# Optimization experiments

Measured on AMD Instinct MI355X. Metric: run time of the kernel, lower is better.

Reference implementation:

```python
import jax, jax.numpy as jnp
import numpy as np
import math

B, T, D = 2, 2048, 1024
H = 16
DH = D // H
DFF = 4096
EPS = 1e-5


def setup_inputs() -> dict:
    key = jax.random.key(0)
    ks = jax.random.split(key, 10)
    x = jax.random.normal(ks[0], (B, T, D), dtype=jnp.float32)
    # bool mask, True above diagonal => masked (matches masked_fill semantics)
    causal_mask = jnp.triu(jnp.ones((T, T), dtype=bool), k=1)
    s = 0.02
    return {
        "x": x,
        "causal_mask": causal_mask,
        "gamma1": jnp.ones((D,), jnp.float32),
        "beta1": jnp.zeros((D,), jnp.float32),
        "wq": jax.random.normal(ks[1], (D, D), jnp.float32) * s,
        "wk": jax.random.normal(ks[2], (D, D), jnp.float32) * s,
        "wv": jax.random.normal(ks[3], (D, D), jnp.float32) * s,
        "wo": jax.random.normal(ks[4], (D, D), jnp.float32) * s,
        "gamma2": jnp.ones((D,), jnp.float32),
        "beta2": jnp.zeros((D,), jnp.float32),
        "w1": jax.random.normal(ks[5], (D, DFF), jnp.float32) * s,
        "b1": jnp.zeros((DFF,), jnp.float32),
        "w2": jax.random.normal(ks[6], (DFF, D), jnp.float32) * s,
        "b2": jnp.zeros((D,), jnp.float32),
    }


def _layer_norm(x, gamma, beta):
    mean = jnp.mean(x, axis=-1, keepdims=True)
    var = jnp.mean((x - mean) ** 2, axis=-1, keepdims=True)
    xhat = (x - mean) / jnp.sqrt(var + EPS)
    return gamma * xhat + beta


def _split_heads(x):
    b, t, d = x.shape
    return x.reshape(b, t, H, DH).transpose(0, 2, 1, 3)  # (B,H,T,Dh)


def reference(x, causal_mask, gamma1, beta1, wq, wk, wv, wo,
              gamma2, beta2, w1, b1, w2, b2):
    # --- attention sublayer (pre-LN) ---
    h = _layer_norm(x, gamma1, beta1)
    q = _split_heads(h @ wq)
    k = _split_heads(h @ wk)
    v = _split_heads(h @ wv)
    scores = jnp.einsum('bhqd,bhkd->bhqk', q, k) / math.sqrt(DH)  # (B,H,T,T)
    scores = jnp.where(causal_mask[None, None, :, :], -jnp.inf, scores)
    attn = jax.nn.softmax(scores, axis=-1)
    out = jnp.einsum('bhqk,bhkd->bhqd', attn, v)
    out = out.transpose(0, 2, 1, 3).reshape(x.shape)  # merge heads
    attn_out = out @ wo
    x = x + attn_out
    # --- FFN sublayer (pre-LN) ---
    h = _layer_norm(x, gamma2, beta2)
    ffn = jax.nn.gelu(h @ w1 + b1, approximate=False) @ w2 + b2
    return x + ffn
```

## Files before the change

### kernel.cpp

```cpp
#include <hip/hip_runtime.h>
#include <hip/hip_bf16.h>
#include <math.h>

#define B_   2
#define T_   2048
#define D_   1024
#define H_   16
#define DH_  64
#define DFF_ 4096
#define NTOK (B_*T_)

typedef __attribute__((ext_vector_type(8))) short short8;
typedef __attribute__((ext_vector_type(4))) float f32x4;

static __device__ __forceinline__ short f2bf(float f) {
    union { __hip_bfloat16 h; short s; } u;
    u.h = __float2bfloat16(f);
    return u.s;
}

static __device__ __forceinline__ f32x4 mfma16(short8 a, short8 b, f32x4 c) {
    return __builtin_amdgcn_mfma_f32_16x16x32_bf16(a, b, c, 0, 0, 0);
}

static __device__ __forceinline__ void gload16(const void* g, void* l) {
    __builtin_amdgcn_global_load_lds(
        (__attribute__((address_space(1))) void*)g,
        (__attribute__((address_space(3))) void*)l, 16, 0, 0);
}

static __device__ __forceinline__ short8 lds_read_sw(const short* base, int row, int kbyte) {
    const int off = (row << 7) + (kbyte ^ ((row & 7) << 4));
    return *reinterpret_cast<const short8*>(reinterpret_cast<const char*>(base) + off);
}

static __device__ __forceinline__ void tc_body(
    const float* __restrict__ src, short* __restrict__ dst,
    int K, int N, float scale, int bx, int by, int t)
{
    __shared__ short tile[64][68];
    const int k0 = by * 64, n0 = bx * 64;
    #pragma unroll
    for (int j = 0; j < 4; ++j) {
        const int i = j * 256 + t;
        const int k = i >> 4, c = i & 15;
        const float4 v = *reinterpret_cast<const float4*>(
            src + (size_t)(k0 + k) * N + n0 + c * 4);
        short4 s4;
        s4.x = f2bf(v.x * scale);
        s4.y = f2bf(v.y * scale);
        s4.z = f2bf(v.z * scale);
        s4.w = f2bf(v.w * scale);
        *reinterpret_cast<short4*>(&tile[k][c * 4]) = s4;
    }
    __syncthreads();
    #pragma unroll
    for (int j = 0; j < 4; ++j) {
        const int i = j * 256 + t;
        const int n = i >> 4, c = i & 15;
        short4 s4;
        s4.x = tile[c * 4 + 0][n];
        s4.y = tile[c * 4 + 1][n];
        s4.z = tile[c * 4 + 2][n];
        s4.w = tile[c * 4 + 3][n];
        *reinterpret_cast<short4*>(dst + (size_t)(n0 + n) * K + k0 + c * 4) = s4;
    }
}

__global__ __launch_bounds__(256) void transpose_cast(
    const float* __restrict__ src, short* __restrict__ dst, int K, int N, float scale)
{
    tc_body(src, dst, K, N, scale, blockIdx.x, blockIdx.y, threadIdx.x);
}

__global__ __launch_bounds__(256) void transpose_cast4(
    const float* __restrict__ s0, const float* __restrict__ s1,
    const float* __restrict__ s2, const float* __restrict__ s3,
    short* __restrict__ d0, short* __restrict__ d1,
    short* __restrict__ d2, short* __restrict__ d3, float scale0)
{
    const int z = blockIdx.z;
    const float* src = (z == 0) ? s0 : (z == 1) ? s1 : (z == 2) ? s2 : s3;
    short*       dst = (z == 0) ? d0 : (z == 1) ? d1 : (z == 2) ? d2 : d3;
    const float scale = (z == 0) ? scale0 : 1.0f;
    tc_body(src, dst, 1024, 1024, scale, blockIdx.x, blockIdx.y, threadIdx.x);
}

__global__ __launch_bounds__(256) void ln_kernel(
    const float* __restrict__ in, const float* __restrict__ gamma,
    const float* __restrict__ beta, short* __restrict__ out)
{
    const int row = blockIdx.x * 4 + (threadIdx.x >> 6);
    const int l = threadIdx.x & 63;
    const float* rp = in + (size_t)row * D_;
    float4 v[4];
    float s = 0.f, sq = 0.f;
    #pragma unroll
    for (int j = 0; j < 4; ++j) {
        v[j] = *reinterpret_cast<const float4*>(rp + j * 256 + l * 4);
        s  += v[j].x + v[j].y + v[j].z + v[j].w;
        sq += v[j].x*v[j].x + v[j].y*v[j].y + v[j].z*v[j].z + v[j].w*v[j].w;
    }
    #pragma unroll
    for (int off = 32; off >= 1; off >>= 1) {
        s  += __shfl_xor(s, off);
        sq += __shfl_xor(sq, off);
    }
    const float mean = s * (1.0f / D_);
    float var = sq * (1.0f / D_) - mean * mean;
    var = fmaxf(var, 0.0f);
    const float rstd = rsqrtf(var + 1e-5f);
    #pragma unroll
    for (int j = 0; j < 4; ++j) {
        const float4 g = *reinterpret_cast<const float4*>(gamma + j * 256 + l * 4);
        const float4 b = *reinterpret_cast<const float4*>(beta  + j * 256 + l * 4);
        short4 o;
        o.x = f2bf(g.x * ((v[j].x - mean) * rstd) + b.x);
        o.y = f2bf(g.y * ((v[j].y - mean) * rstd) + b.y);
        o.z = f2bf(g.z * ((v[j].z - mean) * rstd) + b.z);
        o.w = f2bf(g.w * ((v[j].w - mean) * rstd) + b.w);
        *reinterpret_cast<short4*>(out + (size_t)row * D_ + j * 256 + l * 4) = o;
    }
}

template<int BM, int BN, int EPI>
__global__ __launch_bounds__(512) void gemm_kernel(
    const short* __restrict__ A, const short* __restrict__ Bt,
    void* __restrict__ Cout, const float* __restrict__ resid,
    const float* __restrict__ bias, short* __restrict__ vaux,
    int M, int N, int K, int nbx)
{
    constexpr int MB = BM / 4 / 16;
    constexpr int NB = BN / 2 / 16;
    constexpr int JA = BM / 64;
    constexpr int JB = BN / 64;
    constexpr int J  = JA + JB;
    __shared__ short As[2][BM * 64];
    __shared__ short Bs[2][BN * 64];
    const int t = threadIdx.x;
    const int wid = t >> 6, lane = t & 63;
    const int lr = lane & 15, lk = lane >> 4;
    const int cpx = (int)gridDim.x >> 3;
    const int bid = (int)blockIdx.x;
    const int swz = (bid & 7) * cpx + (bid >> 3);
    const int m0 = (swz / nbx) * BM, n0 = (swz % nbx) * BN;
    const int wrow = (wid >> 1) * (BM / 4);
    const int wcol = (wid & 1) * (BN / 2);

    const char* aSrc[JA];
    const char* bSrc[JB];
    #pragma unroll
    for (int j = 0; j < JA; ++j) {
        const int off = j * 8192 + t * 16;
        const int r   = off >> 7;
        const int cb  = (off & 127) ^ ((r & 7) << 4);
        aSrc[j] = (const char*)(A + (size_t)(m0 + r) * K) + cb;
    }
    #pragma unroll
    for (int j = 0; j < JB; ++j) {
        const int off = j * 8192 + t * 16;
        const int r   = off >> 7;
        const int cb  = (off & 127) ^ ((r & 7) << 4);
        bSrc[j] = (const char*)(Bt + (size_t)(n0 + r) * K) + cb;
    }

    f32x4 acc[MB][NB];
    #pragma unroll
    for (int m = 0; m < MB; ++m)
        #pragma unroll
        for (int n = 0; n < NB; ++n) acc[m][n] = (f32x4){0.f, 0.f, 0.f, 0.f};

    const int NT = K >> 6;

    auto stage = [&](int bufsel, int ktile) {
        const int kb = ktile << 7;
        #pragma unroll
        for (int j = 0; j < JA; ++j)
            gload16(aSrc[j] + kb, (char*)As[bufsel] + j * 8192 + wid * 1024);
        #pragma unroll
        for (int j = 0; j < JB; ++j)
            gload16(bSrc[j] + kb, (char*)Bs[bufsel] + j * 8192 + wid * 1024);
    };
    auto compute = [&](int bufsel) {
        #pragma unroll
        for (int kk = 0; kk < 64; kk += 32) {
            short8 af[MB], bf[NB];
            #pragma unroll
            for (int m = 0; m < MB; ++m)
                af[m] = lds_read_sw(As[bufsel], wrow + m * 16 + lr, (kk + lk * 8) * 2);
            #pragma unroll
            for (int n = 0; n < NB; ++n)
                bf[n] = lds_read_sw(Bs[bufsel], wcol + n * 16 + lr, (kk + lk * 8) * 2);
            #pragma unroll
            for (int m = 0; m < MB; ++m)
                #pragma unroll
                for (int n = 0; n < NB; ++n)
                    acc[m][n] = mfma16(af[m], bf[n], acc[m][n]);
        }
    };

    stage(0, 0);
    stage(1, 1);

    for (int kt = 0; kt < NT - 1; ++kt) {
        asm volatile("s_waitcnt vmcnt(%0)" :: "n"(J) : "memory");
        __builtin_amdgcn_s_barrier();
        compute(kt & 1);
        __builtin_amdgcn_s_barrier();
        if (kt + 2 < NT) stage(kt & 1, kt + 2);
    }
    asm volatile("s_waitcnt vmcnt(0)" ::: "memory");
    __builtin_amdgcn_s_barrier();
    compute((NT - 1) & 1);

    #pragma unroll
    for (int m = 0; m < MB; ++m) {
        #pragma unroll
        for (int n = 0; n < NB; ++n) {
            #pragma unroll
            for (int r = 0; r < 4; ++r) {
                const int gr = m0 + wrow + m * 16 + lk * 4 + r;
                const int gc = n0 + wcol + n * 16 + lr;
                const size_t idx = (size_t)gr * N + gc;
                const float v = acc[m][n][r];
                if constexpr (EPI == 0) {
                    ((short*)Cout)[idx] = f2bf(v);
                } else if constexpr (EPI == 1) {
                    ((float*)Cout)[idx] = resid[idx] + v;
                } else if constexpr (EPI == 2) {
                    const float tt = v + bias[gc];
                    const float z  = 2.3025851f * (tt + 0.044715f * tt * tt * tt);
                    const float e2 = __builtin_amdgcn_exp2f(-z);
                    const float ge = tt * __builtin_amdgcn_rcpf(1.0f + e2);
                    ((short*)Cout)[idx] = f2bf(ge);
                } else if constexpr (EPI == 3) {
                    ((float*)Cout)[idx] = resid[idx] + v + bias[gc];
                } else {
                    if (gc < 2048) {
                        ((short*)Cout)[idx] = f2bf(v);
                    } else {
                        const int hh = (gc - 2048) >> 6, dh = (gc - 2048) & 63;
                        const int bb = gr >> 11, tl = gr & 2047;
                        vaux[((size_t)((bb << 4) + hh) * 64 + dh) * 2048 + tl] = f2bf(v);
                    }
                }
            }
        }
    }
}

static __device__ __forceinline__ void attn_tile(
    const short* Kcur, const short* Vcur, char* pw,
    short8 qf0, short8 qf1, int q0, int kvb, bool diag,
    int lr, int lk, f32x4 (&o)[4], float (&mr)[4], float (&ls)[4])
{
    f32x4 s[4];
    #pragma unroll
    for (int n = 0; n < 4; ++n) s[n] = (f32x4){0.f, 0.f, 0.f, 0.f};
    #pragma unroll
    for (int n = 0; n < 4; ++n) {
        s[n] = mfma16(qf0, lds_read_sw(Kcur, n * 16 + lr, (lk * 8) * 2), s[n]);
        s[n] = mfma16(qf1, lds_read_sw(Kcur, n * 16 + lr, (32 + lk * 8) * 2), s[n]);
    }
    #pragma unroll
    for (int r = 0; r < 4; ++r) {
        const int qg = q0 + lk * 4 + r;
        float v0 = s[0][r], v1 = s[1][r], v2 = s[2][r], v3 = s[3][r];
        if (diag) {
            if (kvb +      lr > qg) v0 = -INFINITY;
            if (kvb + 16 + lr > qg) v1 = -INFINITY;
            if (kvb + 32 + lr > qg) v2 = -INFINITY;
            if (kvb + 48 + lr > qg) v3 = -INFINITY;
        }
        const float mxl = fmaxf(fmaxf(v0, v1), fmaxf(v2, v3));
        if (!__all(mxl <= mr[r] + 8.0f)) {
            float mx = mxl;
            mx = fmaxf(mx, __shfl_xor(mx, 1));
            mx = fmaxf(mx, __shfl_xor(mx, 2));
            mx = fmaxf(mx, __shfl_xor(mx, 4));
            mx = fmaxf(mx, __shfl_xor(mx, 8));
            const float mnew = fmaxf(mr[r], mx);
            const float alpha = __builtin_amdgcn_exp2f(mr[r] - mnew);
            o[0][r] *= alpha; o[1][r] *= alpha; o[2][r] *= alpha; o[3][r] *= alpha;
            ls[r] *= alpha;
            mr[r] = mnew;
        }
        const float p0 = __builtin_amdgcn_exp2f(v0 - mr[r]);
        const float p1 = __builtin_amdgcn_exp2f(v1 - mr[r]);
        const float p2 = __builtin_amdgcn_exp2f(v2 - mr[r]);
        const float p3 = __builtin_amdgcn_exp2f(v3 - mr[r]);
        ls[r] += p0 + p1 + p2 + p3;
        const int prow = lk * 4 + r;
        const int sw = (prow & 7) << 4;
        char* prb = pw + prow * 128;
        *(short*)(prb + (((     lr * 2)) ^ sw)) = f2bf(p0);
        *(short*)(prb + ((32 + lr * 2) ^ sw)) = f2bf(p1);
        *(short*)(prb + ((64 + lr * 2) ^ sw)) = f2bf(p2);
        *(short*)(prb + ((96 + lr * 2) ^ sw)) = f2bf(p3);
    }
    asm volatile("s_waitcnt lgkmcnt(0)" ::: "memory");
    #pragma unroll
    for (int kk = 0; kk < 2; ++kk) {
        const short8 pf = *reinterpret_cast<const short8*>(
            pw + lr * 128 + ((kk * 64 + lk * 16) ^ ((lr & 7) << 4)));
        #pragma unroll
        for (int n = 0; n < 4; ++n)
            o[n] = mfma16(pf, lds_read_sw((const short*)Vcur, n * 16 + lr, (kk * 32 + lk * 8) * 2), o[n]);
    }
}

__global__ __launch_bounds__(256) void attn_kernel(
    const short* __restrict__ qkv, const short* __restrict__ vT,
    short* __restrict__ attn)
{
    __shared__ short Ks[2][4096];
    __shared__ short Vs[2][4096];
    __shared__ short Ps[2][4][1024];
    const int xx = blockIdx.x;
    const int bh = blockIdx.y;
    const int qA = xx, qB = 31 - xx;
    const int b = bh >> 4, h = bh & 15;
    const int t = threadIdx.x;
    const int wid = t >> 6, lane = t & 63;
    const int lr = lane & 15, lk = lane >> 4;
    const int q0A = qA * 64 + wid * 16;
    const int q0B = qB * 64 + wid * 16;

    const short* qrowA = qkv + (size_t)(b * T_ + q0A + lr) * 3072 + h * 64;
    const short8 qfA0 = *reinterpret_cast<const short8*>(qrowA + lk * 8);
    const short8 qfA1 = *reinterpret_cast<const short8*>(qrowA + 32 + lk * 8);
    const short* qrowB = qkv + (size_t)(b * T_ + q0B + lr) * 3072 + h * 64;
    const short8 qfB0 = *reinterpret_cast<const short8*>(qrowB + lk * 8);
    const short8 qfB1 = *reinterpret_cast<const short8*>(qrowB + 32 + lk * 8);
    const short* kbase = qkv + (size_t)b * T_ * 3072 + 1024 + h * 64;
    const short* vbase = vT + (size_t)bh * 64 * T_;

    f32x4 oA[4], oB[4];
    float mrA[4], lsA[4], mrB[4], lsB[4];
    #pragma unroll
    for (int n = 0; n < 4; ++n) {
        oA[n] = (f32x4){0.f, 0.f, 0.f, 0.f};
        oB[n] = (f32x4){0.f, 0.f, 0.f, 0.f};
    }
    #pragma unroll
    for (int r = 0; r < 4; ++r) {
        mrA[r] = -INFINITY; lsA[r] = 0.f;
        mrB[r] = -INFINITY; lsB[r] = 0.f;
    }

    const int nkt = qB + 1;

    #pragma unroll
    for (int j = 0; j < 2; ++j) {
        const int off = j * 4096 + t * 16;
        const int r   = off >> 7;
        const int cb  = (off & 127) ^ ((r & 7) << 4);
        gload16(kbase + (size_t)r * 3072 + (cb >> 1), (char*)Ks[0] + j * 4096 + wid * 1024);
        gload16(vbase + (size_t)r * T_   + (cb >> 1), (char*)Vs[0] + j * 4096 + wid * 1024);
    }
    __syncthreads();

    int cur = 0;
    for (int kt = 0; kt < nkt; ++kt) {
        const int kvb = kt * 64;
        if (kt + 1 < nkt) {
            const int nb = kvb + 64;
            #pragma unroll
            for (int j = 0; j < 2; ++j) {
                const int off = j * 4096 + t * 16;
                const int r   = off >> 7;
                const int cb  = (off & 127) ^ ((r & 7) << 4);
                gload16(kbase + (size_t)(nb + r) * 3072 + (cb >> 1),
                        (char*)Ks[cur ^ 1] + j * 4096 + wid * 1024);
                gload16(vbase + (size_t)r * T_ + nb + (cb >> 1),
                        (char*)Vs[cur ^ 1] + j * 4096 + wid * 1024);
            }
        }

        attn_tile(Ks[cur], Vs[cur], (char*)&Ps[1][wid][0],
                  qfB0, qfB1, q0B, kvb, kt == qB, lr, lk, oB, mrB, lsB);
        if (kt <= qA)
            attn_tile(Ks[cur], Vs[cur], (char*)&Ps[0][wid][0],
                      qfA0, qfA1, q0A, kvb, kt == qA, lr, lk, oA, mrA, lsA);

        __syncthreads();
        cur ^= 1;
    }

    #pragma unroll
    for (int r = 0; r < 4; ++r) {
        float lA = lsA[r], lB = lsB[r];
        lA += __shfl_xor(lA, 1); lB += __shfl_xor(lB, 1);
        lA += __shfl_xor(lA, 2); lB += __shfl_xor(lB, 2);
        lA += __shfl_xor(lA, 4); lB += __shfl_xor(lB, 4);
        lA += __shfl_xor(lA, 8); lB += __shfl_xor(lB, 8);
        const float invA = 1.0f / lA, invB = 1.0f / lB;
        short* opA = attn + (size_t)(b * T_ + q0A + lk * 4 + r) * D_ + h * 64;
        short* opB = attn + (size_t)(b * T_ + q0B + lk * 4 + r) * D_ + h * 64;
        #pragma unroll
        for (int n = 0; n < 4; ++n) {
            opA[n * 16 + lr] = f2bf(oA[n][r] * invA);
            opB[n * 16 + lr] = f2bf(oB[n][r] * invB);
        }
    }
}

extern "C" void kernel_launch(void* const* d_in, const int* in_sizes, int n_in,
                              void* d_out, int out_size, void* d_ws, size_t ws_size,
                              hipStream_t stream)
{
    (void)in_sizes; (void)n_in; (void)out_size; (void)ws_size;
    const float* x      = (const float*)d_in[0];
    const float* gamma1 = (const float*)d_in[2];
    const float* beta1  = (const float*)d_in[3];
    const float* wq     = (const float*)d_in[4];
    const float* wk     = (const float*)d_in[5];
    const float* wv     = (const float*)d_in[6];
    const float* wo     = (const float*)d_in[7];
    const float* gamma2 = (const float*)d_in[8];
    const float* beta2  = (const float*)d_in[9];
    const float* w1     = (const float*)d_in[10];
    const float* b1     = (const float*)d_in[11];
    const float* w2     = (const float*)d_in[12];
    const float* b2     = (const float*)d_in[13];
    float* out = (float*)d_out;

    char* ws = (char*)d_ws;
    size_t off = 0;
    short* wqkvT = (short*)(ws + off); off += (size_t)3072 * 1024 * 2;
    short* woT   = (short*)(ws + off); off += (size_t)1024 * 1024 * 2;
    short* w1T   = (short*)(ws + off); off += (size_t)4096 * 1024 * 2;
    short* w2T   = (short*)(ws + off); off += (size_t)1024 * 4096 * 2;
    short* h1    = (short*)(ws + off); off += (size_t)NTOK * 1024 * 2;
    short* h2    = (short*)(ws + off); off += (size_t)NTOK * 1024 * 2;
    float* y     = (float*)(ws + off); off += (size_t)NTOK * 1024 * 4;
    short* attnb = (short*)(ws + off); off += (size_t)NTOK * 1024 * 2;
    short* qkv   = (short*)(ws + off); off += (size_t)NTOK * 3072 * 2;
    short* vT    = (short*)(ws + off); off += (size_t)B_ * H_ * DH_ * T_ * 2;
    short* g     = qkv;

    transpose_cast4<<<dim3(16, 16, 4), 256, 0, stream>>>(
        wq, wk, wv, wo,
        wqkvT, wqkvT + 1024 * 1024, wqkvT + 2048 * 1024, woT,
        0.18033688011112042f);
    transpose_cast<<<dim3(64, 16), 256, 0, stream>>>(w1, w1T, 1024, 4096, 1.0f);
    transpose_cast<<<dim3(16, 64), 256, 0, stream>>>(w2, w2T, 4096, 1024, 1.0f);

    ln_kernel<<<NTOK / 4, 256, 0, stream>>>(x, gamma1, beta1, h1);

    gemm_kernel<128, 128, 4><<<768, 512, 0, stream>>>(
        h1, wqkvT, qkv, nullptr, nullptr, vT, NTOK, 3072, 1024, 24);

    attn_kernel<<<dim3(16, 32), 256, 0, stream>>>(qkv, vT, attnb);

    gemm_kernel<128, 64, 1><<<512, 512, 0, stream>>>(
        attnb, woT, y, x, nullptr, nullptr, NTOK, 1024, 1024, 16);

    ln_kernel<<<NTOK / 4, 256, 0, stream>>>(y, gamma2, beta2, h2);

    gemm_kernel<128, 128, 2><<<1024, 512, 0, stream>>>(
        h2, w1T, g, nullptr, b1, nullptr, NTOK, 4096, 1024, 32);

    gemm_kernel<128, 64, 3><<<512, 512, 0, stream>>>(
        g, w2T, out, y, b2, nullptr, NTOK, 1024, 4096, 16);
}
```

Before: 247.0 us.

## Add 256x256-tile GEMM kernel for FFN up-projection with fused GELU

Adds a dedicated GEMM kernel for the FFN first layer that uses 256x256 output tiles per 512-thread block (each wave computes 128x64). It splits the A and B staging so the next k-tile's B and A loads are issued between compute phases, and raises wave priority around the MFMA runs. The larger tile raises arithmetic intensity and cuts global traffic per FLOP. In exchange it doubles LDS use to 128KB, holds 32 accumulators per wave, and launches only 256 blocks, which barely covers the CUs. The old EPI 0 and 2 branches are dropped from the generic GEMM.

```diff
diff --git a/kernel.cpp b/kernel.cpp
--- a/kernel.cpp
+++ b/kernel.cpp
@@ -223,16 +223,8 @@
                 const int gc = n0 + wcol + n * 16 + lr;
                 const size_t idx = (size_t)gr * N + gc;
                 const float v = acc[m][n][r];
-                if constexpr (EPI == 0) {
-                    ((short*)Cout)[idx] = f2bf(v);
-                } else if constexpr (EPI == 1) {
+                if constexpr (EPI == 1) {
                     ((float*)Cout)[idx] = resid[idx] + v;
-                } else if constexpr (EPI == 2) {
-                    const float tt = v + bias[gc];
-                    const float z  = 2.3025851f * (tt + 0.044715f * tt * tt * tt);
-                    const float e2 = __builtin_amdgcn_exp2f(-z);
-                    const float ge = tt * __builtin_amdgcn_rcpf(1.0f + e2);
-                    ((short*)Cout)[idx] = f2bf(ge);
                 } else if constexpr (EPI == 3) {
                     ((float*)Cout)[idx] = resid[idx] + v + bias[gc];
                 } else {
@@ -244,6 +236,159 @@
                         vaux[((size_t)((bb << 4) + hh) * 64 + dh) * 2048 + tl] = f2bf(v);
                     }
                 }
+            }
+        }
+    }
+}
+
+__global__ __launch_bounds__(512) void gemm256_kernel(
+    const short* __restrict__ A, const short* __restrict__ Bt,
+    short* __restrict__ Cout, const float* __restrict__ bias,
+    int K, int N, int nbx)
+{
+    __shared__ short As[2][16384];
+    __shared__ short Bs[2][16384];
+    const int t = threadIdx.x;
+    const int wid = t >> 6, lane = t & 63;
+    const int lr = lane & 15, lk = lane >> 4;
+    const int cpx = (int)gridDim.x >> 3;
+    const int bid = (int)blockIdx.x;
+    const int swz = (bid & 7) * cpx + (bid >> 3);
+    const int m0 = (swz / nbx) * 256, n0 = (swz % nbx) * 256;
+    const int wr = (wid >> 2) * 128;
+    const int wc = (wid & 3) * 64;
+
+    const char* aSrc[4];
+    const char* bSrc[4];
+    #pragma unroll
+    for (int j = 0; j < 4; ++j) {
+        const int off = j * 8192 + t * 16;
+        const int r   = off >> 7;
+        const int cb  = (off & 127) ^ ((r & 7) << 4);
+        aSrc[j] = (const char*)(A  + (size_t)(m0 + r) * K) + cb;
+        bSrc[j] = (const char*)(Bt + (size_t)(n0 + r) * K) + cb;
+    }
+
+    f32x4 acc[8][4];
+    #pragma unroll
+    for (int m = 0; m < 8; ++m)
+        #pragma unroll
+        for (int n = 0; n < 4; ++n) acc[m][n] = (f32x4){0.f, 0.f, 0.f, 0.f};
+
+    const int NT = K >> 6;
+
+    auto stageA = [&](int d, int ktile) {
+        const int kb = ktile << 7;
+        #pragma unroll
+        for (int j = 0; j < 4; ++j)
+            gload16(aSrc[j] + kb, (char*)As[d] + j * 8192 + wid * 1024);
+    };
+    auto stageB = [&](int d, int ktile) {
+        const int kb = ktile << 7;
+        #pragma unroll
+        for (int j = 0; j < 4; ++j)
+            gload16(bSrc[j] + kb, (char*)Bs[d] + j * 8192 + wid * 1024);
+    };
+
+    stageA(0, 0); stageB(0, 0);
+    stageB(1, 1); stageA(1, 1);
+
+    for (int kt = 0; kt < NT - 1; ++kt) {
+        const int d = kt & 1;
+        asm volatile("s_waitcnt vmcnt(8)" ::: "memory");
+        __builtin_amdgcn_s_barrier();
+        short8 bf[4][2];
+        #pragma unroll
+        for (int n = 0; n < 4; ++n)
+            #pragma unroll
+            for (int q = 0; q < 2; ++q)
+                bf[n][q] = lds_read_sw(Bs[d], wc + n * 16 + lr, (q * 32 + lk * 8) * 2);
+        {
+            short8 af[2][2];
+            #pragma unroll
+            for (int m = 0; m < 2; ++m)
+                #pragma unroll
+                for (int q = 0; q < 2; ++q)
+                    af[m][q] = lds_read_sw(As[d], wr + m * 16 + lr, (q * 32 + lk * 8) * 2);
+            asm volatile("s_waitcnt lgkmcnt(0)" ::: "memory");
+            __builtin_amdgcn_s_setprio(1);
+            #pragma unroll
+            for (int m = 0; m < 2; ++m)
+                #pragma unroll
+                for (int n = 0; n < 4; ++n)
+                    #pragma unroll
+                    for (int q = 0; q < 2; ++q)
+                        acc[m][n] = mfma16(af[m][q], bf[n][q], acc[m][n]);
+            __builtin_amdgcn_s_setprio(0);
+        }
+        __builtin_amdgcn_s_barrier();
+        if (kt + 2 < NT) stageB(d, kt + 2);
+        #pragma unroll
+        for (int p = 1; p < 4; ++p) {
+            short8 af[2][2];
+            #pragma unroll
+            for (int m = 0; m < 2; ++m)
+                #pragma unroll
+                for (int q = 0; q < 2; ++q)
+                    af[m][q] = lds_read_sw(As[d], wr + (p * 2 + m) * 16 + lr, (q * 32 + lk * 8) * 2);
+            asm volatile("s_waitcnt lgkmcnt(0)" ::: "memory");
+            __builtin_amdgcn_s_setprio(1);
+            #pragma unroll
+            for (int m = 0; m < 2; ++m)
+                #pragma unroll
+                for (int n = 0; n < 4; ++n)
+                    #pragma unroll
+                    for (int q = 0; q < 2; ++q)
+                        acc[p * 2 + m][n] = mfma16(af[m][q], bf[n][q], acc[p * 2 + m][n]);
+            __builtin_amdgcn_s_setprio(0);
+        }
+        __builtin_amdgcn_s_barrier();
+        if (kt + 2 < NT) stageA(d, kt + 2);
+    }
+    {
+        const int d = (NT - 1) & 1;
+        asm volatile("s_waitcnt vmcnt(0)" ::: "memory");
+        __builtin_amdgcn_s_barrier();
+        short8 bf[4][2];
+        #pragma unroll
+        for (int n = 0; n < 4; ++n)
+            #pragma unroll
+            for (int q = 0; q < 2; ++q)
+                bf[n][q] = lds_read_sw(Bs[d], wc + n * 16 + lr, (q * 32 + lk * 8) * 2);
+        #pragma unroll
+        for (int p = 0; p < 4; ++p) {
+            short8 af[2][2];
+            #pragma unroll
+            for (int m = 0; m < 2; ++m)
+                #pragma unroll
+                for (int q = 0; q < 2; ++q)
+                    af[m][q] = lds_read_sw(As[d], wr + (p * 2 + m) * 16 + lr, (q * 32 + lk * 8) * 2);
+            asm volatile("s_waitcnt lgkmcnt(0)" ::: "memory");
+            __builtin_amdgcn_s_setprio(1);
+            #pragma unroll
+            for (int m = 0; m < 2; ++m)
+                #pragma unroll
+                for (int n = 0; n < 4; ++n)
+                    #pragma unroll
+                    for (int q = 0; q < 2; ++q)
+                        acc[p * 2 + m][n] = mfma16(af[m][q], bf[n][q], acc[p * 2 + m][n]);
+            __builtin_amdgcn_s_setprio(0);
+        }
+    }
+
+    #pragma unroll
+    for (int m = 0; m < 8; ++m) {
+        #pragma unroll
+        for (int n = 0; n < 4; ++n) {
+            #pragma unroll
+            for (int r = 0; r < 4; ++r) {
+                const int gr = m0 + wr + m * 16 + lk * 4 + r;
+                const int gc = n0 + wc + n * 16 + lr;
+                const float tt = acc[m][n][r] + bias[gc];
+                const float z  = 2.3025851f * (tt + 0.044715f * tt * tt * tt);
+                const float e2 = __builtin_amdgcn_exp2f(-z);
+                const float ge = tt * __builtin_amdgcn_rcpf(1.0f + e2);
+                Cout[(size_t)gr * N + gc] = f2bf(ge);
             }
         }
     }
@@ -458,8 +603,7 @@
 
     ln_kernel<<<NTOK / 4, 256, 0, stream>>>(y, gamma2, beta2, h2);
 
-    gemm_kernel<128, 128, 2><<<1024, 512, 0, stream>>>(
-        h2, w1T, g, nullptr, b1, nullptr, NTOK, 4096, 1024, 32);
+    gemm256_kernel<<<256, 512, 0, stream>>>(h2, w1T, g, b1, 1024, 4096, 16);
 
     gemm_kernel<128, 64, 3><<<512, 512, 0, stream>>>(
         g, w2T, out, y, b2, nullptr, NTOK, 1024, 4096, 16);
```

New measurement: 239.5 us. 1.03x faster.
